# Kernel optimization log

Measured on AMD Instinct MI355X. Metric: run time of the kernel, lower is better.

## Reference

```python
import jax, jax.numpy as jnp
import numpy as np

VOCAB, EMB_D, RNN_D, HID_D, SEQ = 400000, 50, 512, 1024, 8192


def setup_inputs() -> dict:
    key = jax.random.key(0)
    ks = jax.random.split(key, 9)
    s1 = jax.random.randint(ks[0], (1, SEQ), 0, VOCAB, dtype=jnp.int64)
    s2 = jax.random.randint(ks[1], (1, SEQ), 0, VOCAB, dtype=jnp.int64)
    emb = jax.random.normal(ks[2], (VOCAB, EMB_D), dtype=jnp.float32)
    W_ih = jax.random.normal(ks[3], (RNN_D, EMB_D), dtype=jnp.float32) * 0.05
    W_hh = jax.random.normal(ks[4], (RNN_D, RNN_D), dtype=jnp.float32) * 0.04
    W_hid = jax.random.normal(ks[5], (HID_D, 2 * RNN_D), dtype=jnp.float32) * 0.03
    b_hid = jax.random.normal(ks[6], (HID_D,), dtype=jnp.float32) * 0.01
    W_out = jax.random.normal(ks[7], (1, HID_D), dtype=jnp.float32) * 0.03
    b_out = jax.random.normal(ks[8], (1,), dtype=jnp.float32) * 0.01
    return {"s1": s1, "s2": s2, "emb": emb, "W_ih": W_ih, "W_hh": W_hh,
            "W_hid": W_hid, "b_hid": b_hid, "W_out": W_out, "b_out": b_out}


def _elman_last(x, W_ih, W_hh):
    # x: [T, EMB_D]; vanilla tanh RNN, bias=False; returns last hidden state [RNN_D]
    xp = x @ W_ih.T  # [T, RNN_D], hoist input projection out of the recurrence
    h0 = jnp.zeros((W_hh.shape[0],), dtype=x.dtype)

    def step(h, xt):
        h = jnp.tanh(xt + h @ W_hh.T)
        return h, None

    hT, _ = jax.lax.scan(step, h0, xp)
    return hT


def reference(s1, s2, emb, W_ih, W_hh, W_hid, b_hid, W_out, b_out):
    e1 = emb[s1[0]]  # embedding(s1).squeeze(0) -> [SEQ, EMB_D]
    e2 = emb[s2[0]]
    h1 = _elman_last(e1, W_ih, W_hh)  # rnn_out1[-1, :]
    h2 = _elman_last(e2, W_ih, W_hh)
    cat = jnp.concatenate([h1, h2])[None, :]  # [1, 2*RNN_D]
    hid = jax.nn.relu(cat @ W_hid.T + b_hid)  # dropout is identity in eval mode
    out = jax.nn.sigmoid(hid @ W_out.T + b_out)
    return out[0, 0]
```

## Files before the change

kernel.cpp:

```cpp
#include <hip/hip_runtime.h>
#include <hip/hip_bf16.h>
#include <stdint.h>

#define VOCAB 400000
#define EMB_D 50
#define RNN   512
#define HID   1024
#define SEQ   8192

#define CANARY_BITS 0x40000000u

#define SPIN_CAP 65536

__global__ void k_detect(const unsigned int* s1, const unsigned int* s2,
                         unsigned int* flag) {
    __shared__ unsigned int red[256];
    unsigned int x = 0;
    for (int i = threadIdx.x; i < SEQ / 2; i += 256) {
        x |= s1[2 * i + 1];
        x |= s2[2 * i + 1];
    }
    red[threadIdx.x] = x;
    __syncthreads();
    for (int s = 128; s > 0; s >>= 1) {
        if (threadIdx.x < s) red[threadIdx.x] |= red[threadIdx.x + s];
        __syncthreads();
    }
    if (threadIdx.x == 0) *flag = (red[0] != 0) ? 1u : 0u;
}

__global__ void k_init(float* HA, float* HB) {
    const size_t n = (size_t)(SEQ + 1) * RNN;
    const float canary = __uint_as_float(CANARY_BITS);
    size_t i = (size_t)blockIdx.x * blockDim.x + threadIdx.x;
    const size_t stride = (size_t)gridDim.x * blockDim.x;
    for (; i < n; i += stride) {
        float v = (i < RNN) ? 0.0f : canary;
        HA[i] = v;
        HB[i] = v;
    }
}

__global__ __launch_bounds__(512) void k_xp(const void* s_tok,
                                            const float* __restrict__ emb,
                                            const float* __restrict__ Wih,
                                            float* __restrict__ XP,
                                            const unsigned int* __restrict__ flag) {
    const int tb = blockIdx.x;
    const int r  = threadIdx.x;
    const bool i32 = (*flag != 0);

    float wih[EMB_D];
#pragma unroll
    for (int k = 0; k < EMB_D; ++k) wih[k] = Wih[r * EMB_D + k];

    __shared__ float e[64];

    for (int tt = 0; tt < 64; ++tt) {
        const int t = tb * 64 + tt;
        long long tok;
        if (i32) tok = (long long)((const int*)s_tok)[t];
        else     tok = ((const long long*)s_tok)[t];
        if (r < EMB_D) e[r] = emb[(size_t)tok * EMB_D + r];
        __syncthreads();
        float acc = 0.0f;
#pragma unroll
        for (int k = 0; k < EMB_D; ++k) acc = fmaf(wih[k], e[k], acc);
        XP[(size_t)t * RNN + r] = acc;
        __syncthreads();
    }
}

__global__ __launch_bounds__(512, 2) void rnn_rec(const float* __restrict__ XPA,
                                                  const float* __restrict__ XPB,
                                                  float* HA, float* HB,
                                                  const float* __restrict__ Whh) {
    const int g   = blockIdx.x;
    const int tid = threadIdx.x;
    const int w   = tid >> 6;
    const int l   = tid & 63;
    const int row = g * 64 + l;
    const int colbase = w * 64;

    __shared__ __align__(16) float hs[8][64];
    __shared__ float P[8][64];
    __shared__ float h_ownA[64];
    __shared__ float h_ownB[64];

    float wr[64];
    {
        const float* wp = Whh + (size_t)row * RNN + colbase;
#pragma unroll
        for (int j4 = 0; j4 < 16; ++j4) {
            float4 v = *(const float4*)(wp + 4 * j4);
            wr[4 * j4 + 0] = v.x;
            wr[4 * j4 + 1] = v.y;
            wr[4 * j4 + 2] = v.z;
            wr[4 * j4 + 3] = v.w;
        }
    }

    float xpA_cur = 0.0f, xpB_cur = 0.0f;
    if (w == 0) {
        xpA_cur = XPA[row];
        xpB_cur = XPB[row];
    }

    auto phase = [&](const float* __restrict__ XP, float* H, float* h_own,
                     float& xp_cur, int t) {
        float hv;
        if (w == g && t > 0) {
            hv = h_own[l];
        } else {
            unsigned int u;
            int tries = 0;
            do {
                u = __hip_atomic_load((unsigned int*)&H[(size_t)t * RNN + colbase + l],
                                      __ATOMIC_RELAXED, __HIP_MEMORY_SCOPE_AGENT);
            } while (__any((int)(u == CANARY_BITS)) && ++tries < SPIN_CAP);
            hv = __uint_as_float(u);
        }

        hs[w][l] = hv;
        __builtin_amdgcn_wave_barrier();
        float a0 = 0.0f, a1 = 0.0f, a2 = 0.0f, a3 = 0.0f;
        float4 h4 = *(const float4*)&hs[w][0];
#pragma unroll
        for (int j4 = 0; j4 < 16; ++j4) {
            float4 cur = h4;
            if (j4 < 15) h4 = *(const float4*)&hs[w][4 * (j4 + 1)];
            a0 = fmaf(wr[4 * j4 + 0], cur.x, a0);
            a1 = fmaf(wr[4 * j4 + 1], cur.y, a1);
            a2 = fmaf(wr[4 * j4 + 2], cur.z, a2);
            a3 = fmaf(wr[4 * j4 + 3], cur.w, a3);
        }
        P[w][l] = (a0 + a1) + (a2 + a3);
        __syncthreads();

        if (w == 0) {
            float s = 0.0f;
#pragma unroll
            for (int w2 = 0; w2 < 8; ++w2) s += P[w2][l];
            float hn = tanhf(s + xp_cur);
            __hip_atomic_store((unsigned int*)&H[(size_t)(t + 1) * RNN + g * 64 + l],
                               __float_as_uint(hn),
                               __ATOMIC_RELAXED, __HIP_MEMORY_SCOPE_AGENT);
            h_own[l] = hn;
            const int tn = (t + 1 < SEQ) ? (t + 1) : (SEQ - 1);
            xp_cur = XP[(size_t)tn * RNN + g * 64 + l];
        }
        __syncthreads();
    };

    for (int t = 0; t < SEQ; ++t) {
        phase(XPA, HA, h_ownA, xpA_cur, t);
        phase(XPB, HB, h_ownB, xpB_cur, t);
    }
}

__global__ __launch_bounds__(1024) void k_hid(const float* HA, const float* HB,
                                              const float* __restrict__ Whid,
                                              const float* __restrict__ bhid,
                                              float* __restrict__ hid) {
    __shared__ float cat[2 * RNN];
    const int tid = threadIdx.x;
    cat[tid] = (tid < RNN) ? HA[(size_t)SEQ * RNN + tid]
                           : HB[(size_t)SEQ * RNN + (tid - RNN)];
    __syncthreads();

    const int rl  = tid >> 5;
    const int cl  = tid & 31;
    const int r   = blockIdx.x * 32 + rl;
    float acc = 0.0f;
#pragma unroll
    for (int i = 0; i < 32; ++i) {
        const int c = cl + 32 * i;
        acc = fmaf(Whid[(size_t)r * (2 * RNN) + c], cat[c], acc);
    }
    for (int d = 16; d > 0; d >>= 1) acc += __shfl_down(acc, d, 32);
    if (cl == 0) {
        float h = acc + bhid[r];
        hid[r] = (h > 0.0f) ? h : 0.0f;
    }
}

__global__ __launch_bounds__(1024) void k_out(const float* __restrict__ hid,
                                              const float* __restrict__ Wout,
                                              const float* __restrict__ bout,
                                              float* __restrict__ out) {
    const int tid = threadIdx.x;
    float v = hid[tid] * Wout[tid];
    for (int d = 32; d > 0; d >>= 1) v += __shfl_down(v, d, 64);
    __shared__ float red[16];
    if ((tid & 63) == 0) red[tid >> 6] = v;
    __syncthreads();
    if (tid < 16) {
        float s = red[tid];
        for (int d = 8; d > 0; d >>= 1) s += __shfl_down(s, d, 16);
        if (tid == 0) out[0] = 1.0f / (1.0f + expf(-(s + bout[0])));
    }
}

extern "C" void kernel_launch(void* const* d_in, const int* in_sizes, int n_in,
                              void* d_out, int out_size, void* d_ws, size_t ws_size,
                              hipStream_t stream) {
    const void*  s1   = d_in[0];
    const void*  s2   = d_in[1];
    const float* emb  = (const float*)d_in[2];
    const float* Wih  = (const float*)d_in[3];
    const float* Whh  = (const float*)d_in[4];
    const float* Whid = (const float*)d_in[5];
    const float* bhid = (const float*)d_in[6];
    const float* Wout = (const float*)d_in[7];
    const float* bout = (const float*)d_in[8];
    float* out = (float*)d_out;

    float* XPA  = (float*)d_ws;
    float* XPB  = XPA + (size_t)SEQ * RNN;
    float* HA   = XPB + (size_t)SEQ * RNN;
    float* HB   = HA + (size_t)(SEQ + 1) * RNN;
    float* hid  = HB + (size_t)(SEQ + 1) * RNN;
    unsigned int* flag = (unsigned int*)(hid + HID);

    k_detect<<<1, 256, 0, stream>>>((const unsigned int*)s1,
                                    (const unsigned int*)s2, flag);
    k_init<<<512, 256, 0, stream>>>(HA, HB);
    k_xp<<<SEQ / 64, 512, 0, stream>>>(s1, emb, Wih, XPA, flag);
    k_xp<<<SEQ / 64, 512, 0, stream>>>(s2, emb, Wih, XPB, flag);
    rnn_rec<<<8, 512, 0, stream>>>(XPA, XPB, HA, HB, Whh);
    k_hid<<<HID / 32, 1024, 0, stream>>>(HA, HB, Whid, bhid, hid);
    k_out<<<1, 1024, 0, stream>>>(hid, Wout, bout, out);
}
```

Before: 15.49 ms.

## Co-locate recurrence blocks on one XCC and use sc0 cache-local flag polling

The recurrent kernel now launches 64 blocks. Each block reads its XCC id from a hardware register, and the first XCC to gather eight blocks claims the recurrence; all other blocks exit. Once the eight blocks verify that sc0 (L2-level) loads and stores are visible among themselves, the cross-block hidden-state exchange uses those cheaper accesses instead of agent-scope atomics, which should cut the latency of each step's handoff. The final per-row reduction is also spread across all waves with shuffles instead of wave 0 alone, and the P array is padded. Risks include the election handshake cost, reliance on the XCC hardware register, and correctness depending on the sc0 coherence probe.

```diff
diff --git a/kernel.cpp b/kernel.cpp
--- a/kernel.cpp
+++ b/kernel.cpp
@@ -9,8 +9,21 @@
 #define SEQ   8192
 
 #define CANARY_BITS 0x40000000u
+#define MAGIC       0x5a5a5a5au
 
 #define SPIN_CAP 65536
+
+#define CTL_INTS 128
+
+__device__ __forceinline__ unsigned load_u32_sc0(const unsigned* p) {
+    unsigned v;
+    asm volatile("global_load_dword %0, %1, off sc0\n\ts_waitcnt vmcnt(0)"
+                 : "=v"(v) : "v"(p) : "memory");
+    return v;
+}
+__device__ __forceinline__ void store_u32_sc0(unsigned* p, unsigned v) {
+    asm volatile("global_store_dword %0, %1, off sc0" :: "v"(p), "v"(v) : "memory");
+}
 
 __global__ void k_detect(const unsigned int* s1, const unsigned int* s2,
                          unsigned int* flag) {
@@ -29,7 +42,14 @@
     if (threadIdx.x == 0) *flag = (red[0] != 0) ? 1u : 0u;
 }
 
-__global__ void k_init(float* HA, float* HB) {
+__global__ void k_init(float* HA, float* HB, int* ctl) {
+    if (blockIdx.x == 0 && threadIdx.x < CTL_INTS) {
+        int i = threadIdx.x;
+        int v = 0;
+        if (i == 8) v = -1;
+        if (i == 10) v = 1;
+        ctl[i] = v;
+    }
     const size_t n = (size_t)(SEQ + 1) * RNN;
     const float canary = __uint_as_float(CANARY_BITS);
     size_t i = (size_t)blockIdx.x * blockDim.x + threadIdx.x;
@@ -74,16 +94,72 @@
 __global__ __launch_bounds__(512, 2) void rnn_rec(const float* __restrict__ XPA,
                                                   const float* __restrict__ XPB,
                                                   float* HA, float* HB,
-                                                  const float* __restrict__ Whh) {
-    const int g   = blockIdx.x;
+                                                  const float* __restrict__ Whh,
+                                                  int* ctl) {
+    __shared__ int role_sh, mode_sh;
     const int tid = threadIdx.x;
+
+    if (tid == 0) {
+        unsigned xcc;
+        asm volatile("s_getreg_b32 %0, hwreg(20, 0, 32)" : "=s"(xcc));
+        xcc &= 7u;
+        int idx = __hip_atomic_fetch_add(&ctl[xcc], 1, __ATOMIC_RELAXED,
+                                         __HIP_MEMORY_SCOPE_AGENT);
+        int role = -1, mode = 0;
+        if (idx < 8) {
+            if (idx == 7) {
+                int exp = -1;
+                __hip_atomic_compare_exchange_strong(&ctl[8], &exp, (int)xcc,
+                    __ATOMIC_RELAXED, __ATOMIC_RELAXED, __HIP_MEMORY_SCOPE_AGENT);
+            }
+            int e = -1, sp = 0;
+            do {
+                e = __hip_atomic_load(&ctl[8], __ATOMIC_RELAXED,
+                                      __HIP_MEMORY_SCOPE_AGENT);
+            } while (e < 0 && ++sp < 1000000);
+            if (e == (int)xcc) {
+                role = idx;
+                unsigned* tok = (unsigned*)&ctl[64];
+                store_u32_sc0(&tok[role], MAGIC);
+                int ok = 1;
+                for (int j = 0; j < 8; ++j) {
+                    unsigned v; int sp2 = 0;
+                    do { v = load_u32_sc0(&tok[j]); }
+                    while (v != MAGIC && ++sp2 < SPIN_CAP);
+                    ok &= (v == MAGIC);
+                }
+                __hip_atomic_fetch_and(&ctl[10], ok, __ATOMIC_ACQ_REL,
+                                       __HIP_MEMORY_SCOPE_AGENT);
+                __hip_atomic_fetch_add(&ctl[9], 1, __ATOMIC_ACQ_REL,
+                                       __HIP_MEMORY_SCOPE_AGENT);
+                int c, sp3 = 0;
+                do {
+                    c = __hip_atomic_load(&ctl[9], __ATOMIC_ACQUIRE,
+                                          __HIP_MEMORY_SCOPE_AGENT);
+                } while (c < 8 && ++sp3 < 50000000);
+                if (c >= 8) {
+                    mode = (__hip_atomic_load(&ctl[10], __ATOMIC_ACQUIRE,
+                                              __HIP_MEMORY_SCOPE_AGENT) == 1);
+                } else {
+                    mode = 0;
+                }
+            }
+        }
+        role_sh = role;
+        mode_sh = mode;
+    }
+    __syncthreads();
+    const int g = role_sh;
+    if (g < 0) return;
+    const int mode = mode_sh;
+
     const int w   = tid >> 6;
     const int l   = tid & 63;
     const int row = g * 64 + l;
     const int colbase = w * 64;
 
     __shared__ __align__(16) float hs[8][64];
-    __shared__ float P[8][64];
+    __shared__ float P[8][73];
     __shared__ float h_ownA[64];
     __shared__ float h_ownB[64];
 
@@ -99,25 +175,36 @@
             wr[4 * j4 + 3] = v.w;
         }
     }
+#pragma unroll
+    for (int i = 0; i < 64; ++i) asm volatile("" : "+v"(wr[i]));
 
     float xpA_cur = 0.0f, xpB_cur = 0.0f;
-    if (w == 0) {
-        xpA_cur = XPA[row];
-        xpB_cur = XPB[row];
-    }
-
-    auto phase = [&](const float* __restrict__ XP, float* H, float* h_own,
+    if (l < 8) {
+        xpA_cur = XPA[g * 64 + 8 * w + l];
+        xpB_cur = XPB[g * 64 + 8 * w + l];
+    }
+
+    unsigned* HAu = (unsigned*)HA;
+    unsigned* HBu = (unsigned*)HB;
+
+    auto phase = [&](const float* __restrict__ XP, unsigned* Hu, float* h_own,
                      float& xp_cur, int t) {
         float hv;
         if (w == g && t > 0) {
             hv = h_own[l];
         } else {
-            unsigned int u;
+            unsigned* pp = Hu + (size_t)t * RNN + colbase + l;
+            unsigned u;
             int tries = 0;
-            do {
-                u = __hip_atomic_load((unsigned int*)&H[(size_t)t * RNN + colbase + l],
-                                      __ATOMIC_RELAXED, __HIP_MEMORY_SCOPE_AGENT);
-            } while (__any((int)(u == CANARY_BITS)) && ++tries < SPIN_CAP);
+            if (mode) {
+                do { u = load_u32_sc0(pp); }
+                while (__any((int)(u == CANARY_BITS)) && ++tries < SPIN_CAP);
+            } else {
+                do {
+                    u = __hip_atomic_load(pp, __ATOMIC_RELAXED,
+                                          __HIP_MEMORY_SCOPE_AGENT);
+                } while (__any((int)(u == CANARY_BITS)) && ++tries < SPIN_CAP);
+            }
             hv = __uint_as_float(u);
         }
 
@@ -137,24 +224,28 @@
         P[w][l] = (a0 + a1) + (a2 + a3);
         __syncthreads();
 
-        if (w == 0) {
-            float s = 0.0f;
-#pragma unroll
-            for (int w2 = 0; w2 < 8; ++w2) s += P[w2][l];
-            float hn = tanhf(s + xp_cur);
-            __hip_atomic_store((unsigned int*)&H[(size_t)(t + 1) * RNN + g * 64 + l],
-                               __float_as_uint(hn),
-                               __ATOMIC_RELAXED, __HIP_MEMORY_SCOPE_AGENT);
-            h_own[l] = hn;
+        float v = P[l >> 3][8 * w + (l & 7)];
+        v += __shfl_xor(v, 8);
+        v += __shfl_xor(v, 16);
+        v += __shfl_xor(v, 32);
+        if (l < 8) {
+            const int r = 8 * w + l;
+            float hn = tanhf(v + xp_cur);
+            unsigned ub = __float_as_uint(hn);
+            unsigned* gp = Hu + (size_t)(t + 1) * RNN + g * 64 + r;
+            if (mode) store_u32_sc0(gp, ub);
+            else __hip_atomic_store(gp, ub, __ATOMIC_RELAXED,
+                                    __HIP_MEMORY_SCOPE_AGENT);
+            h_own[r] = hn;
             const int tn = (t + 1 < SEQ) ? (t + 1) : (SEQ - 1);
-            xp_cur = XP[(size_t)tn * RNN + g * 64 + l];
+            xp_cur = XP[(size_t)tn * RNN + g * 64 + r];
         }
         __syncthreads();
     };
 
     for (int t = 0; t < SEQ; ++t) {
-        phase(XPA, HA, h_ownA, xpA_cur, t);
-        phase(XPB, HB, h_ownB, xpB_cur, t);
+        phase(XPA, HAu, h_ownA, xpA_cur, t);
+        phase(XPB, HBu, h_ownB, xpB_cur, t);
     }
 }
 
@@ -168,9 +259,9 @@
                            : HB[(size_t)SEQ * RNN + (tid - RNN)];
     __syncthreads();
 
-    const int rl  = tid >> 5;
-    const int cl  = tid & 31;
-    const int r   = blockIdx.x * 32 + rl;
+    const int rl = tid >> 5;
+    const int cl = tid & 31;
+    const int r  = blockIdx.x * 32 + rl;
     float acc = 0.0f;
 #pragma unroll
     for (int i = 0; i < 32; ++i) {
@@ -215,7 +306,8 @@
     const float* bout = (const float*)d_in[8];
     float* out = (float*)d_out;
 
-    float* XPA  = (float*)d_ws;
+    int* ctl = (int*)d_ws;
+    float* XPA  = (float*)((char*)d_ws + CTL_INTS * sizeof(int));
     float* XPB  = XPA + (size_t)SEQ * RNN;
     float* HA   = XPB + (size_t)SEQ * RNN;
     float* HB   = HA + (size_t)(SEQ + 1) * RNN;
@@ -224,10 +316,10 @@
 
     k_detect<<<1, 256, 0, stream>>>((const unsigned int*)s1,
                                     (const unsigned int*)s2, flag);
-    k_init<<<512, 256, 0, stream>>>(HA, HB);
+    k_init<<<512, 256, 0, stream>>>(HA, HB, ctl);
     k_xp<<<SEQ / 64, 512, 0, stream>>>(s1, emb, Wih, XPA, flag);
     k_xp<<<SEQ / 64, 512, 0, stream>>>(s2, emb, Wih, XPB, flag);
-    rnn_rec<<<8, 512, 0, stream>>>(XPA, XPB, HA, HB, Whh);
+    rnn_rec<<<64, 512, 0, stream>>>(XPA, XPB, HA, HB, Whh, ctl);
     k_hid<<<HID / 32, 1024, 0, stream>>>(HA, HB, Whid, bhid, hid);
     k_out<<<1, 1024, 0, stream>>>(hid, Wout, bout, out);
 }
```

Result: slower. 17.34 ms (+12.0%).
